# Kernel tuning notes

Hardware: AMD Instinct MI355X
Metric: run time of the kernel (lower is better)

## Reference

```python
import jax, jax.numpy as jnp
import numpy as np

D_MODEL = 512
NUM_HEADS = 8
D_K = D_MODEL // NUM_HEADS
B, L = 2, 4096


def setup_inputs() -> dict:
    key = jax.random.key(0)
    ks = jax.random.split(key, 11)
    s = 1.0 / np.sqrt(D_MODEL)
    return {
        "Q": jax.random.normal(ks[0], (B, L, D_MODEL), jnp.float32),
        "K": jax.random.normal(ks[1], (B, L, D_MODEL), jnp.float32),
        "V": jax.random.normal(ks[2], (B, L, D_MODEL), jnp.float32),
        "Wq": jax.random.normal(ks[3], (D_MODEL, D_MODEL), jnp.float32) * s,
        "bq": jax.random.normal(ks[4], (D_MODEL,), jnp.float32) * s,
        "Wk": jax.random.normal(ks[5], (D_MODEL, D_MODEL), jnp.float32) * s,
        "bk": jax.random.normal(ks[6], (D_MODEL,), jnp.float32) * s,
        "Wv": jax.random.normal(ks[7], (D_MODEL, D_MODEL), jnp.float32) * s,
        "bv": jax.random.normal(ks[8], (D_MODEL,), jnp.float32) * s,
        "Wo": jax.random.normal(ks[9], (D_MODEL, D_MODEL), jnp.float32) * s,
        "bo": jax.random.normal(ks[10], (D_MODEL,), jnp.float32) * s,
    }


def reference(Q, K, V, Wq, bq, Wk, bk, Wv, bv, Wo, bo):
    b, l, d = Q.shape
    h, dk = NUM_HEADS, D_K
    # projections: [B, L, D] -> [B, H, L, dk]
    def proj(x, W, bias):
        y = x @ W.T + bias
        return y.reshape(b, l, h, dk).transpose(0, 2, 1, 3)
    q = proj(Q, Wq, bq)
    k = proj(K, Wk, bk)
    v = proj(V, Wv, bv)
    scores = jnp.einsum("bhqd,bhkd->bhqk", q, k) / jnp.sqrt(jnp.float32(dk))
    attn = jax.nn.softmax(scores, axis=-1)
    head_out = jnp.einsum("bhqk,bhkd->bhqd", attn, v)
    out = head_out.transpose(0, 2, 1, 3).reshape(b, l, d)
    return out @ Wo.T + bo
```

## Files before the change

### kernel.cpp

```cpp
#include <hip/hip_runtime.h>

#define SEQ 4096
#define DM 512
#define DK 64
#define NT (SEQ / 64)

typedef __attribute__((ext_vector_type(8))) short bf16x8;
typedef __attribute__((ext_vector_type(4))) short bf16x4;
typedef __attribute__((ext_vector_type(4))) float f32x4;

static __device__ __forceinline__ short bf16rn(float f) {
    unsigned u = __builtin_bit_cast(unsigned, f);
    u = (u + 0x7FFFu + ((u >> 16) & 1u)) >> 16;
    return (short)u;
}

__global__ __launch_bounds__(256) void cvt_w(const float* __restrict__ x, short* __restrict__ y) {
    size_t i = ((size_t)blockIdx.x * 256 + threadIdx.x) * 8;
    float4 a = *(const float4*)(x + i);
    float4 b = *(const float4*)(x + i + 4);
    bf16x8 o;
    o[0] = bf16rn(a.x); o[1] = bf16rn(a.y); o[2] = bf16rn(a.z); o[3] = bf16rn(a.w);
    o[4] = bf16rn(b.x); o[5] = bf16rn(b.y); o[6] = bf16rn(b.z); o[7] = bf16rn(b.w);
    *(bf16x8*)(y + i) = o;
}

template<int MODE>
__global__ __launch_bounds__(256) void gemm_bf16(const void* __restrict__ Xv,
        const short* __restrict__ W, const float* __restrict__ bias, void* __restrict__ Y) {
    __shared__ short Xs[64][72];
    __shared__ short Ws[64][72];
    const int t = threadIdx.x, lane = t & 63, w = t >> 6;
    const int g = lane >> 4, c = lane & 15;
    const int sr = t >> 2, sc = t & 3;
    const int m0 = blockIdx.x << 6, n0 = blockIdx.y << 6;

    f32x4 acc[4] = {};

    for (int k0 = 0; k0 < DM; k0 += 64) {
        if (MODE == 3) {
            const short* px = (const short*)Xv + (size_t)(m0 + sr) * DM + k0 + sc * 16;
            bf16x8 x0 = *(const bf16x8*)px;
            bf16x8 x1 = *(const bf16x8*)(px + 8);
            *(bf16x8*)&Xs[sr][sc * 16]     = x0;
            *(bf16x8*)&Xs[sr][sc * 16 + 8] = x1;
        } else {
            const float* px = (const float*)Xv + (size_t)(m0 + sr) * DM + k0 + sc * 16;
            float4 a = *(const float4*)px;
            float4 b = *(const float4*)(px + 4);
            float4 e = *(const float4*)(px + 8);
            float4 d = *(const float4*)(px + 12);
            bf16x8 x0, x1;
            x0[0] = bf16rn(a.x); x0[1] = bf16rn(a.y); x0[2] = bf16rn(a.z); x0[3] = bf16rn(a.w);
            x0[4] = bf16rn(b.x); x0[5] = bf16rn(b.y); x0[6] = bf16rn(b.z); x0[7] = bf16rn(b.w);
            x1[0] = bf16rn(e.x); x1[1] = bf16rn(e.y); x1[2] = bf16rn(e.z); x1[3] = bf16rn(e.w);
            x1[4] = bf16rn(d.x); x1[5] = bf16rn(d.y); x1[6] = bf16rn(d.z); x1[7] = bf16rn(d.w);
            *(bf16x8*)&Xs[sr][sc * 16]     = x0;
            *(bf16x8*)&Xs[sr][sc * 16 + 8] = x1;
        }
        {
            const short* pw = W + (size_t)(n0 + sr) * DM + k0 + sc * 16;
            bf16x8 w0 = *(const bf16x8*)pw;
            bf16x8 w1 = *(const bf16x8*)(pw + 8);
            *(bf16x8*)&Ws[sr][sc * 16]     = w0;
            *(bf16x8*)&Ws[sr][sc * 16 + 8] = w1;
        }
        __syncthreads();
        #pragma unroll
        for (int kc = 0; kc < 2; ++kc) {
            bf16x8 a8 = *(bf16x8*)&Xs[16 * w + c][32 * kc + 8 * g];
            #pragma unroll
            for (int f = 0; f < 4; ++f) {
                bf16x8 b8 = *(bf16x8*)&Ws[16 * f + c][32 * kc + 8 * g];
                acc[f] = __builtin_amdgcn_mfma_f32_16x16x32_bf16(a8, b8, acc[f], 0, 0, 0);
            }
        }
        __syncthreads();
    }

    float bs[4];
    #pragma unroll
    for (int f = 0; f < 4; ++f) bs[f] = bias[n0 + 16 * f + c];
    const int b = m0 >> 12, h = blockIdx.y;

    if (MODE == 0 || MODE == 1) {
        short* Yp = (short*)Y;
        #pragma unroll
        for (int f = 0; f < 4; ++f) {
            #pragma unroll
            for (int r = 0; r < 4; ++r) {
                int m = m0 + 16 * w + 4 * g + r;
                float val = acc[f][r] + bs[f];
                if (MODE == 0) val *= 0.125f;
                Yp[((size_t)(b * 8 + h) * SEQ + (m & 4095)) * DK + 16 * f + c] = bf16rn(val);
            }
        }
    } else if (MODE == 3) {
        float* Yp = (float*)Y;
        #pragma unroll
        for (int f = 0; f < 4; ++f) {
            #pragma unroll
            for (int r = 0; r < 4; ++r) {
                int m = m0 + 16 * w + 4 * g + r;
                Yp[(size_t)m * DM + n0 + 16 * f + c] = acc[f][r] + bs[f];
            }
        }
    } else {
        short (&Ls)[64][72] = Xs;
        #pragma unroll
        for (int f = 0; f < 4; ++f) {
            #pragma unroll
            for (int r = 0; r < 4; ++r)
                Ls[16 * f + c][16 * w + 4 * g + r] = bf16rn(acc[f][r] + bs[f]);
        }
        __syncthreads();
        short* Yp = (short*)Y;
        bf16x8 r0 = *(bf16x8*)&Ls[sr][sc * 16];
        bf16x8 r1 = *(bf16x8*)&Ls[sr][sc * 16 + 8];
        short* dst = Yp + ((size_t)(b * 8 + h) * DK + sr) * SEQ + (m0 & 4095) + sc * 16;
        *(bf16x8*)dst = r0;
        *(bf16x8*)(dst + 8) = r1;
    }
}

__global__ __launch_bounds__(256) void attn_fwd(const short* __restrict__ qp,
        const short* __restrict__ kp, const short* __restrict__ vtp, short* __restrict__ ho) {
    __shared__ short Ks[64][72];
    __shared__ short Vts[64][72];
    const int t = threadIdx.x, lane = t & 63, w = t >> 6;
    const int g = lane >> 4, c = lane & 15;
    const int sr = t >> 2, sc = t & 3;
    const int q0 = blockIdx.x << 6, bh = blockIdx.y;

    const short* kb  = kp  + (size_t)bh * SEQ * DK;
    const short* vtb = vtp + (size_t)bh * DK * SEQ;

    const short* qrow = qp + ((size_t)bh * SEQ + q0 + 16 * w + c) * DK;
    const bf16x8 qf0 = *(const bf16x8*)(qrow + 8 * g);
    const bf16x8 qf1 = *(const bf16x8*)(qrow + 32 + 8 * g);

    f32x4 o4[4] = {};
    float m_run = -1e30f, l_run = 0.f;

    bf16x8 kr0 = *(const bf16x8*)(kb + (size_t)sr * DK + sc * 16);
    bf16x8 kr1 = *(const bf16x8*)(kb + (size_t)sr * DK + sc * 16 + 8);
    bf16x8 vr0 = *(const bf16x8*)(vtb + (size_t)sr * SEQ + sc * 16);
    bf16x8 vr1 = *(const bf16x8*)(vtb + (size_t)sr * SEQ + sc * 16 + 8);

    for (int kt = 0; kt < NT; ++kt) {
        *(bf16x8*)&Ks[sr][sc * 16]      = kr0;
        *(bf16x8*)&Ks[sr][sc * 16 + 8]  = kr1;
        *(bf16x8*)&Vts[sr][sc * 16]     = vr0;
        *(bf16x8*)&Vts[sr][sc * 16 + 8] = vr1;
        __syncthreads();
        if (kt + 1 < NT) {
            const int kv0 = (kt + 1) << 6;
            kr0 = *(const bf16x8*)(kb + (size_t)(kv0 + sr) * DK + sc * 16);
            kr1 = *(const bf16x8*)(kb + (size_t)(kv0 + sr) * DK + sc * 16 + 8);
            vr0 = *(const bf16x8*)(vtb + (size_t)sr * SEQ + kv0 + sc * 16);
            vr1 = *(const bf16x8*)(vtb + (size_t)sr * SEQ + kv0 + sc * 16 + 8);
        }

        f32x4 s4[4] = {};
        #pragma unroll
        for (int f = 0; f < 4; ++f) {
            bf16x8 a8 = *(bf16x8*)&Ks[16 * f + c][8 * g];
            s4[f] = __builtin_amdgcn_mfma_f32_16x16x32_bf16(a8, qf0, s4[f], 0, 0, 0);
        }
        #pragma unroll
        for (int f = 0; f < 4; ++f) {
            bf16x8 a8 = *(bf16x8*)&Ks[16 * f + c][32 + 8 * g];
            s4[f] = __builtin_amdgcn_mfma_f32_16x16x32_bf16(a8, qf1, s4[f], 0, 0, 0);
        }

        float pm = s4[0][0];
        #pragma unroll
        for (int f = 0; f < 4; ++f) {
            #pragma unroll
            for (int r = 0; r < 4; ++r) pm = fmaxf(pm, s4[f][r]);
        }
        pm = fmaxf(pm, __shfl_xor(pm, 16));
        pm = fmaxf(pm, __shfl_xor(pm, 32));
        const float mnew  = fmaxf(m_run, pm);
        const float alpha = __expf(m_run - mnew);
        float rs = 0.f;
        #pragma unroll
        for (int f = 0; f < 4; ++f) {
            #pragma unroll
            for (int r = 0; r < 4; ++r) {
                float p = __expf(s4[f][r] - mnew);
                s4[f][r] = p;
                rs += p;
            }
        }
        rs += __shfl_xor(rs, 16);
        rs += __shfl_xor(rs, 32);
        l_run = l_run * alpha + rs;
        m_run = mnew;
        #pragma unroll
        for (int fd = 0; fd < 4; ++fd) {
            #pragma unroll
            for (int r = 0; r < 4; ++r) o4[fd][r] *= alpha;
        }

        #pragma unroll
        for (int f = 0; f < 4; ++f) {
            bf16x4 pb = { bf16rn(s4[f][0]), bf16rn(s4[f][1]), bf16rn(s4[f][2]), bf16rn(s4[f][3]) };
            #pragma unroll
            for (int fd = 0; fd < 4; ++fd) {
                bf16x4 va = *(bf16x4*)&Vts[16 * fd + c][16 * f + 4 * g];
                o4[fd] = __builtin_amdgcn_mfma_f32_16x16x16bf16_1k(va, pb, o4[fd], 0, 0, 0);
            }
        }
        __syncthreads();
    }

    const float inv = 1.0f / l_run;
    short (&Ls)[64][72] = Ks;
    #pragma unroll
    for (int fd = 0; fd < 4; ++fd) {
        #pragma unroll
        for (int r = 0; r < 4; ++r)
            Ls[16 * w + c][16 * fd + 4 * g + r] = bf16rn(o4[fd][r] * inv);
    }
    __syncthreads();
    const int b = bh >> 3, h = bh & 7;
    bf16x8 r0 = *(bf16x8*)&Ls[sr][sc * 16];
    bf16x8 r1 = *(bf16x8*)&Ls[sr][sc * 16 + 8];
    short* dst = ho + ((size_t)(b * SEQ + q0 + sr)) * DM + h * DK + sc * 16;
    *(bf16x8*)dst = r0;
    *(bf16x8*)(dst + 8) = r1;
}

extern "C" void kernel_launch(void* const* d_in, const int* in_sizes, int n_in,
                              void* d_out, int out_size, void* d_ws, size_t ws_size,
                              hipStream_t stream) {
    const float* Q  = (const float*)d_in[0];
    const float* K  = (const float*)d_in[1];
    const float* V  = (const float*)d_in[2];
    const float* Wq = (const float*)d_in[3];
    const float* bq = (const float*)d_in[4];
    const float* Wk = (const float*)d_in[5];
    const float* bk = (const float*)d_in[6];
    const float* Wv = (const float*)d_in[7];
    const float* bv = (const float*)d_in[8];
    const float* Wo = (const float*)d_in[9];
    const float* bo = (const float*)d_in[10];

    const size_t NIN = (size_t)2 * SEQ * DM;
    const size_t NW  = (size_t)DM * DM;

    short* wqb  = (short*)d_ws;
    short* wkb  = wqb + NW;
    short* wvb  = wkb + NW;
    short* wob  = wvb + NW;
    short* qws  = wob + NW;
    short* kws  = qws + NIN;
    short* vtws = kws + NIN;
    short* hws  = vtws + NIN;

    cvt_w<<<NW / 2048, 256, 0, stream>>>(Wq, wqb);
    cvt_w<<<NW / 2048, 256, 0, stream>>>(Wk, wkb);
    cvt_w<<<NW / 2048, 256, 0, stream>>>(Wv, wvb);
    cvt_w<<<NW / 2048, 256, 0, stream>>>(Wo, wob);

    dim3 pg(128, 8);
    gemm_bf16<0><<<pg, 256, 0, stream>>>(Q, wqb, bq, qws);
    gemm_bf16<1><<<pg, 256, 0, stream>>>(K, wkb, bk, kws);
    gemm_bf16<2><<<pg, 256, 0, stream>>>(V, wvb, bv, vtws);

    attn_fwd<<<dim3(SEQ / 64, 16), 256, 0, stream>>>(qws, kws, vtws, hws);

    gemm_bf16<3><<<pg, 256, 0, stream>>>(hws, wob, bo, d_out);
}
```

Baseline: 325.5 us.

## Fuse QKV projections, inline weight conversion, use exp2 softmax with lazy rescale

Removes the four weight-conversion kernels and converts fp32 weights to bf16 inside the GEMM tile loads. The three Q/K/V projections are merged into one launch via blockIdx.z. Attention now folds log2(e) into the Q scale so it can use a hardware exp2, and rescales the running max only when it grows by more than 8, which skips most alpha multiplies. The V shared-memory tile is padded to 76 columns to avoid bank conflicts. The trade-off is repeated weight conversion in every block and more conversion work inside the GEMM inner loop.

```diff
diff --git a/kernel.cpp b/kernel.cpp
--- a/kernel.cpp
+++ b/kernel.cpp
@@ -1,4 +1,5 @@
 #include <hip/hip_runtime.h>
+#include <hip/hip_bf16.h>
 
 #define SEQ 4096
 #define DM 512
@@ -9,25 +10,110 @@
 typedef __attribute__((ext_vector_type(4))) short bf16x4;
 typedef __attribute__((ext_vector_type(4))) float f32x4;
 
-static __device__ __forceinline__ short bf16rn(float f) {
-    unsigned u = __builtin_bit_cast(unsigned, f);
-    u = (u + 0x7FFFu + ((u >> 16) & 1u)) >> 16;
-    return (short)u;
-}
-
-__global__ __launch_bounds__(256) void cvt_w(const float* __restrict__ x, short* __restrict__ y) {
-    size_t i = ((size_t)blockIdx.x * 256 + threadIdx.x) * 8;
-    float4 a = *(const float4*)(x + i);
-    float4 b = *(const float4*)(x + i + 4);
-    bf16x8 o;
-    o[0] = bf16rn(a.x); o[1] = bf16rn(a.y); o[2] = bf16rn(a.z); o[3] = bf16rn(a.w);
-    o[4] = bf16rn(b.x); o[5] = bf16rn(b.y); o[6] = bf16rn(b.z); o[7] = bf16rn(b.w);
-    *(bf16x8*)(y + i) = o;
-}
-
-template<int MODE>
-__global__ __launch_bounds__(256) void gemm_bf16(const void* __restrict__ Xv,
-        const short* __restrict__ W, const float* __restrict__ bias, void* __restrict__ Y) {
+#define QSCL 0.18033688011112043f
+
+static __device__ __forceinline__ short bf16h(float f) {
+    union { __hip_bfloat16 h; short s; } u;
+    u.h = __float2bfloat16(f);
+    return u.s;
+}
+
+static __device__ __forceinline__ float fexp2(float x) {
+#if __has_builtin(__builtin_amdgcn_exp2f)
+    return __builtin_amdgcn_exp2f(x);
+#else
+    return exp2f(x);
+#endif
+}
+
+static __device__ __forceinline__ void cvt16(const float* __restrict__ p, short* dst) {
+    float4 a = *(const float4*)p;
+    float4 b = *(const float4*)(p + 4);
+    float4 e = *(const float4*)(p + 8);
+    float4 d = *(const float4*)(p + 12);
+    bf16x8 x0, x1;
+    x0[0] = bf16h(a.x); x0[1] = bf16h(a.y); x0[2] = bf16h(a.z); x0[3] = bf16h(a.w);
+    x0[4] = bf16h(b.x); x0[5] = bf16h(b.y); x0[6] = bf16h(b.z); x0[7] = bf16h(b.w);
+    x1[0] = bf16h(e.x); x1[1] = bf16h(e.y); x1[2] = bf16h(e.z); x1[3] = bf16h(e.w);
+    x1[4] = bf16h(d.x); x1[5] = bf16h(d.y); x1[6] = bf16h(d.z); x1[7] = bf16h(d.w);
+    *(bf16x8*)dst = x0;
+    *(bf16x8*)(dst + 8) = x1;
+}
+
+__global__ __launch_bounds__(256) void proj_qkv(
+        const float* __restrict__ Qx, const float* __restrict__ Kx, const float* __restrict__ Vx,
+        const float* __restrict__ Wq, const float* __restrict__ Wk, const float* __restrict__ Wv,
+        const float* __restrict__ bq, const float* __restrict__ bk, const float* __restrict__ bv,
+        short* __restrict__ qo, short* __restrict__ ko, short* __restrict__ vo) {
+    __shared__ short Xs[64][72];
+    __shared__ short Ws[64][72];
+    const int z = blockIdx.z;
+    const float* X    = z == 0 ? Qx : z == 1 ? Kx : Vx;
+    const float* W    = z == 0 ? Wq : z == 1 ? Wk : Wv;
+    const float* bias = z == 0 ? bq : z == 1 ? bk : bv;
+
+    const int t = threadIdx.x, lane = t & 63, w = t >> 6;
+    const int g = lane >> 4, c = lane & 15;
+    const int sr = t >> 2, sc = t & 3;
+    const int m0 = blockIdx.x << 6, n0 = blockIdx.y << 6;
+
+    f32x4 acc[4] = {};
+    const float* px = X + (size_t)(m0 + sr) * DM + sc * 16;
+    const float* pw = W + (size_t)(n0 + sr) * DM + sc * 16;
+
+    for (int k0 = 0; k0 < DM; k0 += 64) {
+        cvt16(px, &Xs[sr][sc * 16]);
+        cvt16(pw, &Ws[sr][sc * 16]);
+        px += 64; pw += 64;
+        __syncthreads();
+        #pragma unroll
+        for (int kc = 0; kc < 2; ++kc) {
+            bf16x8 a8 = *(bf16x8*)&Xs[16 * w + c][32 * kc + 8 * g];
+            #pragma unroll
+            for (int f = 0; f < 4; ++f) {
+                bf16x8 b8 = *(bf16x8*)&Ws[16 * f + c][32 * kc + 8 * g];
+                acc[f] = __builtin_amdgcn_mfma_f32_16x16x32_bf16(a8, b8, acc[f], 0, 0, 0);
+            }
+        }
+        __syncthreads();
+    }
+
+    float bs[4];
+    #pragma unroll
+    for (int f = 0; f < 4; ++f) bs[f] = bias[n0 + 16 * f + c];
+    const int b = m0 >> 12, h = blockIdx.y;
+
+    if (z == 0 || z == 1) {
+        short* Yp = z == 0 ? qo : ko;
+        const float scl = z == 0 ? QSCL : 1.0f;
+        #pragma unroll
+        for (int f = 0; f < 4; ++f) {
+            #pragma unroll
+            for (int r = 0; r < 4; ++r) {
+                int m = m0 + 16 * w + 4 * g + r;
+                Yp[((size_t)(b * 8 + h) * SEQ + (m & 4095)) * DK + 16 * f + c] =
+                    bf16h((acc[f][r] + bs[f]) * scl);
+            }
+        }
+    } else {
+        short (&Ls)[64][72] = Xs;
+        #pragma unroll
+        for (int f = 0; f < 4; ++f) {
+            #pragma unroll
+            for (int r = 0; r < 4; ++r)
+                Ls[16 * f + c][16 * w + 4 * g + r] = bf16h(acc[f][r] + bs[f]);
+        }
+        __syncthreads();
+        bf16x8 r0 = *(bf16x8*)&Ls[sr][sc * 16];
+        bf16x8 r1 = *(bf16x8*)&Ls[sr][sc * 16 + 8];
+        short* dst = vo + ((size_t)(b * 8 + h) * DK + sr) * SEQ + (m0 & 4095) + sc * 16;
+        *(bf16x8*)dst = r0;
+        *(bf16x8*)(dst + 8) = r1;
+    }
+}
+
+__global__ __launch_bounds__(256) void proj_out(const short* __restrict__ Xb,
+        const float* __restrict__ W, const float* __restrict__ bias, float* __restrict__ Y) {
     __shared__ short Xs[64][72];
     __shared__ short Ws[64][72];
     const int t = threadIdx.x, lane = t & 63, w = t >> 6;
@@ -36,35 +122,14 @@
     const int m0 = blockIdx.x << 6, n0 = blockIdx.y << 6;
 
     f32x4 acc[4] = {};
+    const short* px = Xb + (size_t)(m0 + sr) * DM + sc * 16;
+    const float* pw = W + (size_t)(n0 + sr) * DM + sc * 16;
 
     for (int k0 = 0; k0 < DM; k0 += 64) {
-        if (MODE == 3) {
-            const short* px = (const short*)Xv + (size_t)(m0 + sr) * DM + k0 + sc * 16;
-            bf16x8 x0 = *(const bf16x8*)px;
-            bf16x8 x1 = *(const bf16x8*)(px + 8);
-            *(bf16x8*)&Xs[sr][sc * 16]     = x0;
-            *(bf16x8*)&Xs[sr][sc * 16 + 8] = x1;
-        } else {
-            const float* px = (const float*)Xv + (size_t)(m0 + sr) * DM + k0 + sc * 16;
-            float4 a = *(const float4*)px;
-            float4 b = *(const float4*)(px + 4);
-            float4 e = *(const float4*)(px + 8);
-            float4 d = *(const float4*)(px + 12);
-            bf16x8 x0, x1;
-            x0[0] = bf16rn(a.x); x0[1] = bf16rn(a.y); x0[2] = bf16rn(a.z); x0[3] = bf16rn(a.w);
-            x0[4] = bf16rn(b.x); x0[5] = bf16rn(b.y); x0[6] = bf16rn(b.z); x0[7] = bf16rn(b.w);
-            x1[0] = bf16rn(e.x); x1[1] = bf16rn(e.y); x1[2] = bf16rn(e.z); x1[3] = bf16rn(e.w);
-            x1[4] = bf16rn(d.x); x1[5] = bf16rn(d.y); x1[6] = bf16rn(d.z); x1[7] = bf16rn(d.w);
-            *(bf16x8*)&Xs[sr][sc * 16]     = x0;
-            *(bf16x8*)&Xs[sr][sc * 16 + 8] = x1;
-        }
-        {
-            const short* pw = W + (size_t)(n0 + sr) * DM + k0 + sc * 16;
-            bf16x8 w0 = *(const bf16x8*)pw;
-            bf16x8 w1 = *(const bf16x8*)(pw + 8);
-            *(bf16x8*)&Ws[sr][sc * 16]     = w0;
-            *(bf16x8*)&Ws[sr][sc * 16 + 8] = w1;
-        }
+        *(bf16x8*)&Xs[sr][sc * 16]     = *(const bf16x8*)px;
+        *(bf16x8*)&Xs[sr][sc * 16 + 8] = *(const bf16x8*)(px + 8);
+        cvt16(pw, &Ws[sr][sc * 16]);
+        px += 64; pw += 64;
         __syncthreads();
         #pragma unroll
         for (int kc = 0; kc < 2; ++kc) {
@@ -78,87 +143,61 @@
         __syncthreads();
     }
 
-    float bs[4];
     #pragma unroll
-    for (int f = 0; f < 4; ++f) bs[f] = bias[n0 + 16 * f + c];
-    const int b = m0 >> 12, h = blockIdx.y;
-
-    if (MODE == 0 || MODE == 1) {
-        short* Yp = (short*)Y;
-        #pragma unroll
-        for (int f = 0; f < 4; ++f) {
-            #pragma unroll
-            for (int r = 0; r < 4; ++r) {
-                int m = m0 + 16 * w + 4 * g + r;
-                float val = acc[f][r] + bs[f];
-                if (MODE == 0) val *= 0.125f;
-                Yp[((size_t)(b * 8 + h) * SEQ + (m & 4095)) * DK + 16 * f + c] = bf16rn(val);
-            }
-        }
-    } else if (MODE == 3) {
-        float* Yp = (float*)Y;
-        #pragma unroll
-        for (int f = 0; f < 4; ++f) {
-            #pragma unroll
-            for (int r = 0; r < 4; ++r) {
-                int m = m0 + 16 * w + 4 * g + r;
-                Yp[(size_t)m * DM + n0 + 16 * f + c] = acc[f][r] + bs[f];
-            }
-        }
-    } else {
-        short (&Ls)[64][72] = Xs;
-        #pragma unroll
-        for (int f = 0; f < 4; ++f) {
-            #pragma unroll
-            for (int r = 0; r < 4; ++r)
-                Ls[16 * f + c][16 * w + 4 * g + r] = bf16rn(acc[f][r] + bs[f]);
-        }
-        __syncthreads();
-        short* Yp = (short*)Y;
-        bf16x8 r0 = *(bf16x8*)&Ls[sr][sc * 16];
-        bf16x8 r1 = *(bf16x8*)&Ls[sr][sc * 16 + 8];
-        short* dst = Yp + ((size_t)(b * 8 + h) * DK + sr) * SEQ + (m0 & 4095) + sc * 16;
-        *(bf16x8*)dst = r0;
-        *(bf16x8*)(dst + 8) = r1;
+    for (int f = 0; f < 4; ++f) {
+        float bs = bias[n0 + 16 * f + c];
+        #pragma unroll
+        for (int r = 0; r < 4; ++r) {
+            int m = m0 + 16 * w + 4 * g + r;
+            Y[(size_t)m * DM + n0 + 16 * f + c] = acc[f][r] + bs;
+        }
     }
 }
 
 __global__ __launch_bounds__(256) void attn_fwd(const short* __restrict__ qp,
         const short* __restrict__ kp, const short* __restrict__ vtp, short* __restrict__ ho) {
     __shared__ short Ks[64][72];
-    __shared__ short Vts[64][72];
+    __shared__ short Vts[64][76];
     const int t = threadIdx.x, lane = t & 63, w = t >> 6;
     const int g = lane >> 4, c = lane & 15;
     const int sr = t >> 2, sc = t & 3;
     const int q0 = blockIdx.x << 6, bh = blockIdx.y;
 
-    const short* kb  = kp  + (size_t)bh * SEQ * DK;
-    const short* vtb = vtp + (size_t)bh * DK * SEQ;
-
     const short* qrow = qp + ((size_t)bh * SEQ + q0 + 16 * w + c) * DK;
     const bf16x8 qf0 = *(const bf16x8*)(qrow + 8 * g);
     const bf16x8 qf1 = *(const bf16x8*)(qrow + 32 + 8 * g);
 
     f32x4 o4[4] = {};
-    float m_run = -1e30f, l_run = 0.f;
-
-    bf16x8 kr0 = *(const bf16x8*)(kb + (size_t)sr * DK + sc * 16);
-    bf16x8 kr1 = *(const bf16x8*)(kb + (size_t)sr * DK + sc * 16 + 8);
-    bf16x8 vr0 = *(const bf16x8*)(vtb + (size_t)sr * SEQ + sc * 16);
-    bf16x8 vr1 = *(const bf16x8*)(vtb + (size_t)sr * SEQ + sc * 16 + 8);
+    float m_run = -3.0e38f, l_run = 0.f;
+
+    const short* kptr = kp + (size_t)bh * SEQ * DK + (size_t)sr * DK + sc * 16;
+    const short* vptr = vtp + (size_t)bh * DK * SEQ + (size_t)sr * SEQ + sc * 16;
+    bf16x8 kr0 = *(const bf16x8*)kptr;
+    bf16x8 kr1 = *(const bf16x8*)(kptr + 8);
+    bf16x8 vr0 = *(const bf16x8*)vptr;
+    bf16x8 vr1 = *(const bf16x8*)(vptr + 8);
 
     for (int kt = 0; kt < NT; ++kt) {
-        *(bf16x8*)&Ks[sr][sc * 16]      = kr0;
-        *(bf16x8*)&Ks[sr][sc * 16 + 8]  = kr1;
-        *(bf16x8*)&Vts[sr][sc * 16]     = vr0;
-        *(bf16x8*)&Vts[sr][sc * 16 + 8] = vr1;
+        *(bf16x8*)&Ks[sr][sc * 16]     = kr0;
+        *(bf16x8*)&Ks[sr][sc * 16 + 8] = kr1;
+        {
+            bf16x4 t0 = {vr0[0], vr0[1], vr0[2], vr0[3]};
+            bf16x4 t1 = {vr0[4], vr0[5], vr0[6], vr0[7]};
+            bf16x4 t2 = {vr1[0], vr1[1], vr1[2], vr1[3]};
+            bf16x4 t3 = {vr1[4], vr1[5], vr1[6], vr1[7]};
+            *(bf16x4*)&Vts[sr][sc * 16]      = t0;
+            *(bf16x4*)&Vts[sr][sc * 16 + 4]  = t1;
+            *(bf16x4*)&Vts[sr][sc * 16 + 8]  = t2;
+            *(bf16x4*)&Vts[sr][sc * 16 + 12] = t3;
+        }
         __syncthreads();
         if (kt + 1 < NT) {
-            const int kv0 = (kt + 1) << 6;
-            kr0 = *(const bf16x8*)(kb + (size_t)(kv0 + sr) * DK + sc * 16);
-            kr1 = *(const bf16x8*)(kb + (size_t)(kv0 + sr) * DK + sc * 16 + 8);
-            vr0 = *(const bf16x8*)(vtb + (size_t)sr * SEQ + kv0 + sc * 16);
-            vr1 = *(const bf16x8*)(vtb + (size_t)sr * SEQ + kv0 + sc * 16 + 8);
+            kptr += 64 * DK;
+            vptr += 64;
+            kr0 = *(const bf16x8*)kptr;
+            kr1 = *(const bf16x8*)(kptr + 8);
+            vr0 = *(const bf16x8*)vptr;
+            vr1 = *(const bf16x8*)(vptr + 8);
         }
 
         f32x4 s4[4] = {};
@@ -181,31 +220,36 @@
         }
         pm = fmaxf(pm, __shfl_xor(pm, 16));
         pm = fmaxf(pm, __shfl_xor(pm, 32));
-        const float mnew  = fmaxf(m_run, pm);
-        const float alpha = __expf(m_run - mnew);
+
+        if (__any(pm > m_run + 8.0f)) {
+            float mnew  = fmaxf(m_run, pm);
+            float alpha = fexp2(m_run - mnew);
+            l_run *= alpha;
+            #pragma unroll
+            for (int fd = 0; fd < 4; ++fd) {
+                #pragma unroll
+                for (int r = 0; r < 4; ++r) o4[fd][r] *= alpha;
+            }
+            m_run = mnew;
+        }
+
         float rs = 0.f;
         #pragma unroll
         for (int f = 0; f < 4; ++f) {
             #pragma unroll
             for (int r = 0; r < 4; ++r) {
-                float p = __expf(s4[f][r] - mnew);
+                float p = fexp2(s4[f][r] - m_run);
                 s4[f][r] = p;
                 rs += p;
             }
         }
         rs += __shfl_xor(rs, 16);
         rs += __shfl_xor(rs, 32);
-        l_run = l_run * alpha + rs;
-        m_run = mnew;
-        #pragma unroll
-        for (int fd = 0; fd < 4; ++fd) {
-            #pragma unroll
-            for (int r = 0; r < 4; ++r) o4[fd][r] *= alpha;
-        }
-
-        #pragma unroll
-        for (int f = 0; f < 4; ++f) {
-            bf16x4 pb = { bf16rn(s4[f][0]), bf16rn(s4[f][1]), bf16rn(s4[f][2]), bf16rn(s4[f][3]) };
+        l_run += rs;
+
+        #pragma unroll
+        for (int f = 0; f < 4; ++f) {
+            bf16x4 pb = { bf16h(s4[f][0]), bf16h(s4[f][1]), bf16h(s4[f][2]), bf16h(s4[f][3]) };
             #pragma unroll
             for (int fd = 0; fd < 4; ++fd) {
                 bf16x4 va = *(bf16x4*)&Vts[16 * fd + c][16 * f + 4 * g];
@@ -221,7 +265,7 @@
     for (int fd = 0; fd < 4; ++fd) {
         #pragma unroll
         for (int r = 0; r < 4; ++r)
-            Ls[16 * w + c][16 * fd + 4 * g + r] = bf16rn(o4[fd][r] * inv);
+            Ls[16 * w + c][16 * fd + 4 * g + r] = bf16h(o4[fd][r] * inv);
     }
     __syncthreads();
     const int b = bh >> 3, h = bh & 7;
@@ -248,28 +292,14 @@
     const float* bo = (const float*)d_in[10];
 
     const size_t NIN = (size_t)2 * SEQ * DM;
-    const size_t NW  = (size_t)DM * DM;
-
-    short* wqb  = (short*)d_ws;
-    short* wkb  = wqb + NW;
-    short* wvb  = wkb + NW;
-    short* wob  = wvb + NW;
-    short* qws  = wob + NW;
+
+    short* qws  = (short*)d_ws;
     short* kws  = qws + NIN;
     short* vtws = kws + NIN;
     short* hws  = vtws + NIN;
 
-    cvt_w<<<NW / 2048, 256, 0, stream>>>(Wq, wqb);
-    cvt_w<<<NW / 2048, 256, 0, stream>>>(Wk, wkb);
-    cvt_w<<<NW / 2048, 256, 0, stream>>>(Wv, wvb);
-    cvt_w<<<NW / 2048, 256, 0, stream>>>(Wo, wob);
-
-    dim3 pg(128, 8);
-    gemm_bf16<0><<<pg, 256, 0, stream>>>(Q, wqb, bq, qws);
-    gemm_bf16<1><<<pg, 256, 0, stream>>>(K, wkb, bk, kws);
-    gemm_bf16<2><<<pg, 256, 0, stream>>>(V, wvb, bv, vtws);
-
+    proj_qkv<<<dim3(128, 8, 3), 256, 0, stream>>>(Q, K, V, Wq, Wk, Wv, bq, bk, bv,
+                                                  qws, kws, vtws);
     attn_fwd<<<dim3(SEQ / 64, 16), 256, 0, stream>>>(qws, kws, vtws, hws);
-
-    gemm_bf16<3><<<pg, 256, 0, stream>>>(hws, wob, bo, d_out);
-}
+    proj_out<<<dim3(128, 8), 256, 0, stream>>>(hws, Wo, bo, (float*)d_out);
+}
```

New measurement: 293.0 us. 1.11x faster.
